# Kernel tuning notes

Measured on AMD Instinct MI355X. Metric: run time of the kernel, lower is better.

The kernel has to match this reference:

```python
import jax, jax.numpy as jnp
import numpy as np

N_NODES = 32768
N_EDGES = 262144
B = 64
FT_IN = 256
HID = 256
HEADS = 4
C = HID // HEADS
FT_OUT = 256
NEG_SLOPE = 0.2


def _lin(k, fi, fo):
    return jax.random.normal(k, (fi, fo), dtype=jnp.float32) / np.sqrt(fi)


def setup_inputs() -> dict:
    key = jax.random.key(0)
    ks = jax.random.split(key, 20)
    x = jax.random.normal(ks[0], (N_NODES, FT_IN), dtype=jnp.float32)
    edge_index = jax.random.randint(ks[1], (2, N_EDGES), 0, N_NODES, dtype=jnp.int64)
    batch = jnp.repeat(jnp.arange(B, dtype=jnp.int64), N_NODES // B)  # sorted segment ids
    return {
        "x": x,
        "edge_index": edge_index,
        "batch": batch,
        "batch_size": B,
        "W1l": _lin(ks[2], FT_IN, HID),
        "W1r": _lin(ks[3], FT_IN, HID),
        "a1": jax.random.normal(ks[4], (HEADS, C), dtype=jnp.float32) / np.sqrt(C),
        "b1": jnp.zeros((HID,), dtype=jnp.float32),
        "W2l": _lin(ks[5], HID, HID),
        "W2r": _lin(ks[6], HID, HID),
        "a2": jax.random.normal(ks[7], (HEADS, C), dtype=jnp.float32) / np.sqrt(C),
        "b2": jnp.zeros((HID,), dtype=jnp.float32),
        "Wm1": _lin(ks[8], HID, 4 * HID),
        "bm1": jnp.zeros((4 * HID,), dtype=jnp.float32),
        "Wm2": _lin(ks[9], 4 * HID, HID),
        "bm2": jnp.zeros((HID,), dtype=jnp.float32),
        "Wf": _lin(ks[10], HID, FT_OUT),
        "bf": jnp.zeros((FT_OUT,), dtype=jnp.float32),
    }


def gatv2_layer(x, src, dst, Wl, Wr, att, bias):
    """PyG GATv2Conv (concat=True, add_self_loops=True, eval-mode dropout)."""
    n = x.shape[0]
    h, c = att.shape
    xl = (x @ Wl).reshape(n, h, c)  # source-side transform (x_j)
    xr = (x @ Wr).reshape(n, h, c)  # target-side transform (x_i)
    loop = jnp.arange(n, dtype=src.dtype)
    s = jnp.concatenate([src, loop])
    d = jnp.concatenate([dst, loop])
    # e_ij = a^T LeakyReLU(Wl x_j + Wr x_i), per head
    e = jax.nn.leaky_relu(xl[s] + xr[d], NEG_SLOPE)  # [E+N, H, C]
    score = jnp.einsum('ehc,hc->eh', e, att)  # [E+N, H]
    # segment softmax over incoming edges of each dst node
    m = jax.ops.segment_max(score, d, num_segments=n)
    ex = jnp.exp(score - m[d])
    denom = jax.ops.segment_sum(ex, d, num_segments=n)
    alpha = ex / denom[d]  # self-loops guarantee denom > 0
    out = jax.ops.segment_sum(alpha[..., None] * xl[s], d, num_segments=n)
    return out.reshape(n, h * c) + bias


def _gelu(x):
    return jax.nn.gelu(x, approximate=False)


def reference(x, edge_index, batch, batch_size,
              W1l, W1r, a1, b1, W2l, W2r, a2, b2,
              Wm1, bm1, Wm2, bm2, Wf, bf):
    src, dst = edge_index[0], edge_index[1]
    h = _gelu(gatv2_layer(x, src, dst, W1l, W1r, a1, b1))
    h = _gelu(gatv2_layer(h, src, dst, W2l, W2r, a2, b2))
    # global mean pool over graphs
    cnt = jax.ops.segment_sum(jnp.ones((h.shape[0],), h.dtype), batch, num_segments=batch_size)
    graph_mean = jax.ops.segment_sum(h, batch, num_segments=batch_size) / cnt[:, None]
    # root node of each graph (node 0 of each contiguous block)
    root = h.reshape(batch_size, -1, h.shape[-1])[:, 0, :]
    z = _gelu(root @ Wm1 + bm1)
    z = _gelu(z @ Wm2 + bm2)
    out = z @ Wf + bf
    return (out, graph_mean)
```

## Files before the change

kernel.cpp:

```cpp
#include <hip/hip_runtime.h>
#include <math.h>

#define NNODES 32768
#define BGRAPH 64
#define NPG 512
#define HID 256

typedef __bf16 bf16x8 __attribute__((ext_vector_type(8)));
typedef float f32x16 __attribute__((ext_vector_type(16)));
typedef unsigned short ushort_t;
typedef unsigned short ushort8v __attribute__((ext_vector_type(8)));
typedef unsigned short ushort4v __attribute__((ext_vector_type(4)));
typedef _Float16 half4v __attribute__((ext_vector_type(4)));

__device__ __forceinline__ float gelu_f(float x) {
  return 0.5f * x * (1.0f + erff(x * 0.70710678118654752440f));
}

__device__ __forceinline__ int swz_off(int r, int k) {
  int kblk = k & ~63;
  int ch = (k >> 3) & 7;
  int slot = ch ^ (r & 7);
  return r * 256 + kblk + (slot << 3) + (k & 7);
}

__device__ __forceinline__ size_t frag_off(int r, int k) {
  return ((size_t)((r >> 5) * 16 + (k >> 4)) << 9) +
         (size_t)(((r & 31) | (((k >> 3) & 1) << 5)) << 3) + (k & 7);
}

__device__ __forceinline__ void gll16(const void* g, void* l) {
  __builtin_amdgcn_global_load_lds(
      (const __attribute__((address_space(1))) unsigned int*)g,
      (__attribute__((address_space(3))) unsigned int*)l, 16, 0, 0);
}

__device__ __forceinline__ float dpp_sum16(float x) {
  int t;
  t = __builtin_amdgcn_update_dpp(0, __builtin_bit_cast(int, x), 0xB1, 0xF, 0xF, true);
  x += __builtin_bit_cast(float, t);
  t = __builtin_amdgcn_update_dpp(0, __builtin_bit_cast(int, x), 0x4E, 0xF, 0xF, true);
  x += __builtin_bit_cast(float, t);
  t = __builtin_amdgcn_update_dpp(0, __builtin_bit_cast(int, x), 0x141, 0xF, 0xF, true);
  x += __builtin_bit_cast(float, t);
  t = __builtin_amdgcn_update_dpp(0, __builtin_bit_cast(int, x), 0x140, 0xF, 0xF, true);
  x += __builtin_bit_cast(float, t);
  return x;
}

__global__ __launch_bounds__(256) void prep_kernel(
    const int* __restrict__ src, const int* __restrict__ dst, int E,
    int* __restrict__ cnt, ushort_t* __restrict__ col_pad,
    const float* __restrict__ W1l, const float* __restrict__ W1r,
    const float* __restrict__ W2l, const float* __restrict__ W2r,
    ushort_t* __restrict__ B1h, ushort_t* __restrict__ B1l,
    ushort_t* __restrict__ B2h, ushort_t* __restrict__ B2l,
    const float* __restrict__ x,
    ushort_t* __restrict__ Xh, ushort_t* __restrict__ Xl) {
  int b = blockIdx.x;
  if (b < 1024) {
    int e = b * 256 + threadIdx.x;
    if (e < E) {
      int d = dst[e];
      int slot = atomicAdd(&cnt[d], 1);
      if (slot < 64) col_pad[(d << 6) | slot] = (ushort_t)src[e];
    }
  } else if (b < 1152) {
    int idx = (b - 1024) * 256 + threadIdx.x;
    int layer = idx >> 14;
    int n = (idx >> 5) & 511;
    int c32 = idx & 31;
    const float* W = layer ? (n < 256 ? W2l : W2r) : (n < 256 ? W1l : W1r);
    int wn = n & 255;
    ushort8v hv, lv;
#pragma unroll
    for (int j = 0; j < 8; ++j) {
      float v = W[(size_t)(c32 * 8 + j) * 256 + wn];
      __bf16 h = (__bf16)v;
      float rem = v - (float)h;
      __bf16 l = (__bf16)rem;
      hv[j] = __builtin_bit_cast(ushort_t, h);
      lv[j] = __builtin_bit_cast(ushort_t, l);
    }
    size_t off = frag_off(n, c32 * 8);
    ushort_t* ho = layer ? B2h : B1h;
    ushort_t* lo = layer ? B2l : B1l;
    *(ushort8v*)(ho + off) = hv;
    *(ushort8v*)(lo + off) = lv;
  } else {
    int idx = (b - 1152) * 256 + threadIdx.x;
    int r = idx >> 5;
    int c32 = idx & 31;
    const float* srcp = x + (size_t)r * 256 + c32 * 8;
    float4 v0 = *(const float4*)srcp;
    float4 v1 = *(const float4*)(srcp + 4);
    float vv[8] = {v0.x, v0.y, v0.z, v0.w, v1.x, v1.y, v1.z, v1.w};
    ushort8v hv, lv;
#pragma unroll
    for (int j = 0; j < 8; ++j) {
      __bf16 h = (__bf16)vv[j];
      float rem = vv[j] - (float)h;
      __bf16 l = (__bf16)rem;
      hv[j] = __builtin_bit_cast(ushort_t, h);
      lv[j] = __builtin_bit_cast(ushort_t, l);
    }
    int off = swz_off(r, c32 * 8);
    *(ushort8v*)(Xh + off) = hv;
    *(ushort8v*)(Xl + off) = lv;
  }
}

__global__ __launch_bounds__(256, 3) void gemm_bf16x3(
    const ushort_t* __restrict__ Ahi, const ushort_t* __restrict__ Alo,
    const ushort_t* __restrict__ Bhi, const ushort_t* __restrict__ Blo,
    _Float16* __restrict__ Cl, float* __restrict__ Cr) {
  __shared__ ushort_t lds[2 * 8192];
  int i = blockIdx.x;
  int xcd = i & 7, slot = i >> 3;
  int bm = (xcd * 32 + (slot >> 2)) * 128;
  int bn = (slot & 3) * 128;

  int tid = threadIdx.x;
  int w = tid >> 6, lane = tid & 63;
  int wm0 = (w >> 1) * 64, wn0 = (w & 1) * 64;
  int r = lane & 31, kg = lane >> 5;
  int cb0 = (bn + wn0) >> 5;

  f32x16 acc[2][2];
#pragma unroll
  for (int mf = 0; mf < 2; ++mf)
#pragma unroll
    for (int nf = 0; nf < 2; ++nf)
#pragma unroll
      for (int e = 0; e < 16; ++e) acc[mf][nf][e] = 0.0f;

  for (int kk = 0; kk < 256; kk += 64) {
#pragma unroll
    for (int t = 0; t < 8; ++t) {
      int tile = t >> 2;
      int q = tid + (t & 3) * 256;
      const ushort_t* gsrc = tile ? Alo : Ahi;
      gll16(gsrc + (size_t)(bm + (q >> 3)) * 256 + kk + (q & 7) * 8,
            lds + tile * 8192 + q * 8);
    }
    __syncthreads();

    int kq0 = kk >> 4;
#pragma unroll
    for (int ks = 0; ks < 4; ++ks) {
      int so = (((ks << 1) | kg) ^ (r & 7)) << 3;
      bf16x8 ah[2], al[2], bh[2], bl[2];
#pragma unroll
      for (int mf = 0; mf < 2; ++mf) {
        int rb = (wm0 + mf * 32 + r) * 64 + so;
        ah[mf] = *(const bf16x8*)(lds + rb);
        al[mf] = *(const bf16x8*)(lds + 8192 + rb);
      }
#pragma unroll
      for (int nf = 0; nf < 2; ++nf) {
        size_t o = ((size_t)((cb0 + nf) * 16 + kq0 + ks) << 9) + (lane << 3);
        bh[nf] = *(const bf16x8*)(Bhi + o);
        bl[nf] = *(const bf16x8*)(Blo + o);
      }
#pragma unroll
      for (int mf = 0; mf < 2; ++mf)
#pragma unroll
        for (int nf = 0; nf < 2; ++nf) {
          acc[mf][nf] = __builtin_amdgcn_mfma_f32_32x32x16_bf16(ah[mf], bh[nf], acc[mf][nf], 0, 0, 0);
          acc[mf][nf] = __builtin_amdgcn_mfma_f32_32x32x16_bf16(ah[mf], bl[nf], acc[mf][nf], 0, 0, 0);
          acc[mf][nf] = __builtin_amdgcn_mfma_f32_32x32x16_bf16(al[mf], bh[nf], acc[mf][nf], 0, 0, 0);
        }
    }
    __syncthreads();
  }

#pragma unroll
  for (int mf = 0; mf < 2; ++mf)
#pragma unroll
    for (int nf = 0; nf < 2; ++nf) {
      int colbase = bn + wn0 + nf * 32;
      int cn = (colbase + r) & 255;
#pragma unroll
      for (int g = 0; g < 16; ++g) {
        int row = bm + wm0 + mf * 32 + (g & 3) + ((g >> 2) << 3) + (kg << 2);
        if (colbase < 256)
          Cl[(size_t)row * 256 + cn] = (_Float16)acc[mf][nf][g];
        else
          Cr[(size_t)row * 256 + cn] = acc[mf][nf][g];
      }
    }
}

__global__ __launch_bounds__(256) void gat_agg(const _Float16* __restrict__ xl,
                                               const float* __restrict__ xr,
                                               const float* __restrict__ att,
                                               const float* __restrict__ bias,
                                               const int* __restrict__ cnt,
                                               const ushort_t* __restrict__ col_pad,
                                               ushort_t* __restrict__ hi_out,
                                               ushort_t* __restrict__ lo_out,
                                               _Float16* __restrict__ h2f16,
                                               float* __restrict__ rootbuf) {
  int wave = (int)((blockIdx.x * (size_t)blockDim.x + threadIdx.x) >> 6);
  int lane = threadIdx.x & 63;
  int d = wave;
  int c0 = lane * 4;
  float4 xr4 = *(const float4*)(xr + (size_t)d * HID + c0);
  float4 a4 = *(const float4*)(att + c0);
  int deg = cnt[d];
  deg = deg < 64 ? deg : 64;
  int mycol = (int)col_pad[(d << 6) + lane];

  auto loadrow = [&](int j) -> float4 {
    int s = (j < deg) ? __builtin_amdgcn_readlane(mycol, j) : d;
    half4v hv = *(const half4v*)(xl + (size_t)s * HID + c0);
    return make_float4((float)hv[0], (float)hv[1], (float)hv[2], (float)hv[3]);
  };

  float l = 0.f, A0 = 0.f, A1 = 0.f, A2 = 0.f, A3 = 0.f;
  float4 v = loadrow(0);
  for (int j = 0; j <= deg; ++j) {
    float4 vc = v;
    if (j < deg) v = loadrow(j + 1);
    float t0 = vc.x + xr4.x, t1 = vc.y + xr4.y, t2 = vc.z + xr4.z, t3 = vc.w + xr4.w;
    t0 = fmaf(0.4f, fabsf(t0), 0.6f * t0);
    t1 = fmaf(0.4f, fabsf(t1), 0.6f * t1);
    t2 = fmaf(0.4f, fabsf(t2), 0.6f * t2);
    t3 = fmaf(0.4f, fabsf(t3), 0.6f * t3);
    float sc = a4.x * t0;
    sc = fmaf(a4.y, t1, sc);
    sc = fmaf(a4.z, t2, sc);
    sc = fmaf(a4.w, t3, sc);
    sc = dpp_sum16(sc);
    float p = __expf(sc);
    l += p;
    A0 = fmaf(p, vc.x, A0);
    A1 = fmaf(p, vc.y, A1);
    A2 = fmaf(p, vc.z, A2);
    A3 = fmaf(p, vc.w, A3);
  }

  float inv = 1.0f / l;
  float v0 = gelu_f(fmaf(A0, inv, bias[c0 + 0]));
  float v1 = gelu_f(fmaf(A1, inv, bias[c0 + 1]));
  float v2 = gelu_f(fmaf(A2, inv, bias[c0 + 2]));
  float v3 = gelu_f(fmaf(A3, inv, bias[c0 + 3]));

  if (hi_out) {
    float vv[4] = {v0, v1, v2, v3};
    ushort4v hv, lv;
#pragma unroll
    for (int j = 0; j < 4; ++j) {
      __bf16 h = (__bf16)vv[j];
      float rem = vv[j] - (float)h;
      __bf16 lb = (__bf16)rem;
      hv[j] = __builtin_bit_cast(ushort_t, h);
      lv[j] = __builtin_bit_cast(ushort_t, lb);
    }
    int off = swz_off(d, c0);
    *(ushort4v*)(hi_out + off) = hv;
    *(ushort4v*)(lo_out + off) = lv;
  }
  if (h2f16) {
    half4v o;
    o[0] = (_Float16)v0; o[1] = (_Float16)v1; o[2] = (_Float16)v2; o[3] = (_Float16)v3;
    *(half4v*)(h2f16 + (size_t)d * HID + c0) = o;
    if ((d & (NPG - 1)) == 0)
      *(float4*)(rootbuf + (size_t)(d >> 9) * HID + c0) = make_float4(v0, v1, v2, v3);
  }
}

__global__ __launch_bounds__(1024) void pool_kernel(const _Float16* __restrict__ h2,
                                                    float* __restrict__ gmean) {
  __shared__ float buf[1024];
  int g = blockIdx.x;
  int q = threadIdx.x >> 8;
  int c = threadIdx.x & 255;
  const _Float16* p = h2 + ((size_t)g * NPG + q * 128) * HID + c;
  float s = 0.f;
#pragma unroll 4
  for (int i = 0; i < 128; ++i) s += (float)p[(size_t)i * HID];
  buf[threadIdx.x] = s;
  __syncthreads();
  if (threadIdx.x < 256) {
    float tot = buf[c] + buf[256 + c] + buf[512 + c] + buf[768 + c];
    gmean[(size_t)g * HID + c] = tot * (1.0f / (float)NPG);
  }
}

__global__ __launch_bounds__(256) void mlp1_kernel(const float* __restrict__ in,
                                                   const float* __restrict__ W,
                                                   const float* __restrict__ b,
                                                   float* __restrict__ outp) {
  __shared__ float s_in[256];
  int g = blockIdx.x >> 2;
  int n0 = (blockIdx.x & 3) * 256;
  const float* row = in + (size_t)g * 256;
  s_in[threadIdx.x] = row[threadIdx.x];
  __syncthreads();
  float acc = 0.f;
  for (int k = 0; k < 256; ++k)
    acc = fmaf(s_in[k], W[(size_t)k * 1024 + n0 + threadIdx.x], acc);
  outp[(size_t)g * 1024 + n0 + threadIdx.x] = gelu_f(acc + b[n0 + threadIdx.x]);
}

__global__ __launch_bounds__(256) void mlp23_kernel(const float* __restrict__ z1,
                                                    const float* __restrict__ Wm2,
                                                    const float* __restrict__ bm2,
                                                    const float* __restrict__ Wf,
                                                    const float* __restrict__ bf,
                                                    float* __restrict__ outp) {
  __shared__ float s1[1024];
  __shared__ float s2[256];
  int g = blockIdx.x;
  int c = threadIdx.x;
  const float* row = z1 + (size_t)g * 1024;
#pragma unroll
  for (int i = 0; i < 4; ++i) s1[c + i * 256] = row[c + i * 256];
  __syncthreads();
  float acc = 0.f;
  for (int k = 0; k < 1024; ++k) acc = fmaf(s1[k], Wm2[(size_t)k * 256 + c], acc);
  s2[c] = gelu_f(acc + bm2[c]);
  __syncthreads();
  float acc2 = 0.f;
  for (int k = 0; k < 256; ++k) acc2 = fmaf(s2[k], Wf[(size_t)k * 256 + c], acc2);
  outp[(size_t)g * 256 + c] = acc2 + bf[c];
}

extern "C" void kernel_launch(void* const* d_in, const int* in_sizes, int n_in,
                              void* d_out, int out_size, void* d_ws, size_t ws_size,
                              hipStream_t stream) {
  const float* x   = (const float*)d_in[0];
  const int* edge  = (const int*)d_in[1];
  const float* W1l = (const float*)d_in[4];
  const float* W1r = (const float*)d_in[5];
  const float* a1  = (const float*)d_in[6];
  const float* b1  = (const float*)d_in[7];
  const float* W2l = (const float*)d_in[8];
  const float* W2r = (const float*)d_in[9];
  const float* a2  = (const float*)d_in[10];
  const float* b2  = (const float*)d_in[11];
  const float* Wm1 = (const float*)d_in[12];
  const float* bm1 = (const float*)d_in[13];
  const float* Wm2 = (const float*)d_in[14];
  const float* bm2 = (const float*)d_in[15];
  const float* Wf  = (const float*)d_in[16];
  const float* bf  = (const float*)d_in[17];
  float* out = (float*)d_out;
  float* gmean = out + BGRAPH * HID;

  const int n = NNODES;
  const int E = in_sizes[1] / 2;
  const int* src = edge;
  const int* dst = edge + E;

  ushort_t* R1h = (ushort_t*)d_ws;
  ushort_t* R1l = R1h + (size_t)n * 256;
  _Float16* h2f16 = (_Float16*)R1h;
  _Float16* xlh = (_Float16*)(R1l + (size_t)n * 256);
  float* xrbuf = (float*)(xlh + (size_t)n * 256);
  float* rootbuf = xrbuf + (size_t)n * 256;
  float* z1 = rootbuf + 64 * 256;
  ushort_t* B1h = (ushort_t*)(z1 + 64 * 1024);
  ushort_t* B1l = B1h + 512 * 256;
  ushort_t* B2h = B1l + 512 * 256;
  ushort_t* B2l = B2h + 512 * 256;
  int* cnt = (int*)(B2l + 512 * 256);
  ushort_t* col_pad = (ushort_t*)(cnt + n);

  hipMemsetAsync(cnt, 0, (size_t)n * sizeof(int), stream);

  prep_kernel<<<1024 + 128 + 4096, 256, 0, stream>>>(
      src, dst, E, cnt, col_pad, W1l, W1r, W2l, W2r,
      B1h, B1l, B2h, B2l, x, R1h, R1l);

  gemm_bf16x3<<<1024, 256, 0, stream>>>(R1h, R1l, B1h, B1l, xlh, xrbuf);
  gat_agg<<<n / 4, 256, 0, stream>>>(xlh, xrbuf, a1, b1, cnt, col_pad,
                                     R1h, R1l, nullptr, nullptr);
  gemm_bf16x3<<<1024, 256, 0, stream>>>(R1h, R1l, B2h, B2l, xlh, xrbuf);
  gat_agg<<<n / 4, 256, 0, stream>>>(xlh, xrbuf, a2, b2, cnt, col_pad,
                                     nullptr, nullptr, h2f16, rootbuf);

  pool_kernel<<<BGRAPH, 1024, 0, stream>>>(h2f16, gmean);
  mlp1_kernel<<<BGRAPH * 4, 256, 0, stream>>>(rootbuf, Wm1, bm1, z1);
  mlp23_kernel<<<BGRAPH, 256, 0, stream>>>(z1, Wm2, bm2, Wf, bf, out);
}
```

Before: 336.6 us.

## Rewrite MLP head as wave-per-output dot products over transposed weights

Transposes the MLP weight matrices in the prep kernel so each output column is a contiguous row. The MLP head is then computed as three kernels with one wavefront per output, each doing a vectorized float4 dot product and a DPP/shuffle reduction. Previously a single thread looped serially over K, and mlp23 ran only 64 blocks, which left most of the GPU idle. The change costs an extra transpose pass over about 2 MB of weights inside prep and one more kernel launch.

```diff
diff --git a/kernel.cpp b/kernel.cpp
--- a/kernel.cpp
+++ b/kernel.cpp
@@ -48,6 +48,13 @@
   return x;
 }
 
+__device__ __forceinline__ float wave_sum64(float x) {
+  x = dpp_sum16(x);
+  x += __shfl_xor(x, 16);
+  x += __shfl_xor(x, 32);
+  return x;
+}
+
 __global__ __launch_bounds__(256) void prep_kernel(
     const int* __restrict__ src, const int* __restrict__ dst, int E,
     int* __restrict__ cnt, ushort_t* __restrict__ col_pad,
@@ -56,7 +63,10 @@
     ushort_t* __restrict__ B1h, ushort_t* __restrict__ B1l,
     ushort_t* __restrict__ B2h, ushort_t* __restrict__ B2l,
     const float* __restrict__ x,
-    ushort_t* __restrict__ Xh, ushort_t* __restrict__ Xl) {
+    ushort_t* __restrict__ Xh, ushort_t* __restrict__ Xl,
+    const float* __restrict__ Wm1, const float* __restrict__ Wm2,
+    const float* __restrict__ Wf,
+    float* __restrict__ W1T, float* __restrict__ W2T, float* __restrict__ WfT) {
   int b = blockIdx.x;
   if (b < 1024) {
     int e = b * 256 + threadIdx.x;
@@ -87,7 +97,7 @@
     ushort_t* lo = layer ? B2l : B1l;
     *(ushort8v*)(ho + off) = hv;
     *(ushort8v*)(lo + off) = lv;
-  } else {
+  } else if (b < 5248) {
     int idx = (b - 1152) * 256 + threadIdx.x;
     int r = idx >> 5;
     int c32 = idx & 31;
@@ -107,6 +117,18 @@
     int off = swz_off(r, c32 * 8);
     *(ushort8v*)(Xh + off) = hv;
     *(ushort8v*)(Xl + off) = lv;
+  } else if (b < 6272) {
+    int idx = (b - 5248) * 256 + threadIdx.x;
+    int k = idx & 255, n = idx >> 8;
+    W1T[(size_t)n * 256 + k] = Wm1[(size_t)k * 1024 + n];
+  } else if (b < 7296) {
+    int idx = (b - 6272) * 256 + threadIdx.x;
+    int k = idx & 1023, c = idx >> 10;
+    W2T[(size_t)c * 1024 + k] = Wm2[(size_t)k * 256 + c];
+  } else {
+    int idx = (b - 7296) * 256 + threadIdx.x;
+    int k = idx & 255, n = idx >> 8;
+    WfT[(size_t)n * 256 + k] = Wf[(size_t)k * 256 + n];
   }
 }
 
@@ -288,43 +310,61 @@
   }
 }
 
-__global__ __launch_bounds__(256) void mlp1_kernel(const float* __restrict__ in,
-                                                   const float* __restrict__ W,
-                                                   const float* __restrict__ b,
-                                                   float* __restrict__ outp) {
-  __shared__ float s_in[256];
-  int g = blockIdx.x >> 2;
-  int n0 = (blockIdx.x & 3) * 256;
-  const float* row = in + (size_t)g * 256;
-  s_in[threadIdx.x] = row[threadIdx.x];
-  __syncthreads();
-  float acc = 0.f;
-  for (int k = 0; k < 256; ++k)
-    acc = fmaf(s_in[k], W[(size_t)k * 1024 + n0 + threadIdx.x], acc);
-  outp[(size_t)g * 1024 + n0 + threadIdx.x] = gelu_f(acc + b[n0 + threadIdx.x]);
-}
-
-__global__ __launch_bounds__(256) void mlp23_kernel(const float* __restrict__ z1,
-                                                    const float* __restrict__ Wm2,
-                                                    const float* __restrict__ bm2,
-                                                    const float* __restrict__ Wf,
-                                                    const float* __restrict__ bf,
-                                                    float* __restrict__ outp) {
-  __shared__ float s1[1024];
-  __shared__ float s2[256];
-  int g = blockIdx.x;
-  int c = threadIdx.x;
-  const float* row = z1 + (size_t)g * 1024;
-#pragma unroll
-  for (int i = 0; i < 4; ++i) s1[c + i * 256] = row[c + i * 256];
-  __syncthreads();
-  float acc = 0.f;
-  for (int k = 0; k < 1024; ++k) acc = fmaf(s1[k], Wm2[(size_t)k * 256 + c], acc);
-  s2[c] = gelu_f(acc + bm2[c]);
-  __syncthreads();
-  float acc2 = 0.f;
-  for (int k = 0; k < 256; ++k) acc2 = fmaf(s2[k], Wf[(size_t)k * 256 + c], acc2);
-  outp[(size_t)g * 256 + c] = acc2 + bf[c];
+__global__ __launch_bounds__(256) void head1(const float* __restrict__ root,
+                                             const float* __restrict__ W1T,
+                                             const float* __restrict__ b1m,
+                                             float* __restrict__ z1) {
+  int wv = (int)((blockIdx.x * 256 + threadIdx.x) >> 6);
+  int lane = threadIdx.x & 63;
+  int g = wv >> 10, nx = wv & 1023;
+  float4 r = *(const float4*)(root + (size_t)g * 256 + lane * 4);
+  float4 w = *(const float4*)(W1T + (size_t)nx * 256 + lane * 4);
+  float p = r.x * w.x;
+  p = fmaf(r.y, w.y, p);
+  p = fmaf(r.z, w.z, p);
+  p = fmaf(r.w, w.w, p);
+  p = wave_sum64(p);
+  if (lane == 0) z1[(size_t)g * 1024 + nx] = gelu_f(p + b1m[nx]);
+}
+
+__global__ __launch_bounds__(256) void head2(const float* __restrict__ z1,
+                                             const float* __restrict__ W2T,
+                                             const float* __restrict__ b2m,
+                                             float* __restrict__ z2) {
+  int wv = (int)((blockIdx.x * 256 + threadIdx.x) >> 6);
+  int lane = threadIdx.x & 63;
+  int g = wv >> 8, c = wv & 255;
+  const float* zr = z1 + (size_t)g * 1024;
+  const float* wr = W2T + (size_t)c * 1024;
+  float p = 0.f;
+#pragma unroll
+  for (int i = 0; i < 4; ++i) {
+    float4 a = *(const float4*)(zr + i * 256 + lane * 4);
+    float4 w = *(const float4*)(wr + i * 256 + lane * 4);
+    p = fmaf(a.x, w.x, p);
+    p = fmaf(a.y, w.y, p);
+    p = fmaf(a.z, w.z, p);
+    p = fmaf(a.w, w.w, p);
+  }
+  p = wave_sum64(p);
+  if (lane == 0) z2[(size_t)g * 256 + c] = gelu_f(p + b2m[c]);
+}
+
+__global__ __launch_bounds__(256) void head3(const float* __restrict__ z2,
+                                             const float* __restrict__ WfT,
+                                             const float* __restrict__ bfm,
+                                             float* __restrict__ outp) {
+  int wv = (int)((blockIdx.x * 256 + threadIdx.x) >> 6);
+  int lane = threadIdx.x & 63;
+  int g = wv >> 8, nx = wv & 255;
+  float4 a = *(const float4*)(z2 + (size_t)g * 256 + lane * 4);
+  float4 w = *(const float4*)(WfT + (size_t)nx * 256 + lane * 4);
+  float p = a.x * w.x;
+  p = fmaf(a.y, w.y, p);
+  p = fmaf(a.z, w.z, p);
+  p = fmaf(a.w, w.w, p);
+  p = wave_sum64(p);
+  if (lane == 0) outp[(size_t)g * 256 + nx] = p + bfm[nx];
 }
 
 extern "C" void kernel_launch(void* const* d_in, const int* in_sizes, int n_in,
@@ -361,18 +401,23 @@
   float* xrbuf = (float*)(xlh + (size_t)n * 256);
   float* rootbuf = xrbuf + (size_t)n * 256;
   float* z1 = rootbuf + 64 * 256;
-  ushort_t* B1h = (ushort_t*)(z1 + 64 * 1024);
+  float* z2 = z1 + 64 * 1024;
+  ushort_t* B1h = (ushort_t*)(z2 + 64 * 256);
   ushort_t* B1l = B1h + 512 * 256;
   ushort_t* B2h = B1l + 512 * 256;
   ushort_t* B2l = B2h + 512 * 256;
   int* cnt = (int*)(B2l + 512 * 256);
   ushort_t* col_pad = (ushort_t*)(cnt + n);
+  float* W1T = (float*)(col_pad + (size_t)n * 64);
+  float* W2T = W1T + 1024 * 256;
+  float* WfT = W2T + 256 * 1024;
 
   hipMemsetAsync(cnt, 0, (size_t)n * sizeof(int), stream);
 
-  prep_kernel<<<1024 + 128 + 4096, 256, 0, stream>>>(
+  prep_kernel<<<7552, 256, 0, stream>>>(
       src, dst, E, cnt, col_pad, W1l, W1r, W2l, W2r,
-      B1h, B1l, B2h, B2l, x, R1h, R1l);
+      B1h, B1l, B2h, B2l, x, R1h, R1l,
+      Wm1, Wm2, Wf, W1T, W2T, WfT);
 
   gemm_bf16x3<<<1024, 256, 0, stream>>>(R1h, R1l, B1h, B1l, xlh, xrbuf);
   gat_agg<<<n / 4, 256, 0, stream>>>(xlh, xrbuf, a1, b1, cnt, col_pad,
@@ -382,6 +427,7 @@
                                      nullptr, nullptr, h2f16, rootbuf);
 
   pool_kernel<<<BGRAPH, 1024, 0, stream>>>(h2f16, gmean);
-  mlp1_kernel<<<BGRAPH * 4, 256, 0, stream>>>(rootbuf, Wm1, bm1, z1);
-  mlp23_kernel<<<BGRAPH, 256, 0, stream>>>(z1, Wm2, bm2, Wf, bf, out);
-}
+  head1<<<BGRAPH * 1024 / 4, 256, 0, stream>>>(rootbuf, W1T, bm1, z1);
+  head2<<<BGRAPH * 256 / 4, 256, 0, stream>>>(z1, W2T, bm2, z2);
+  head3<<<BGRAPH * 256 / 4, 256, 0, stream>>>(z2, WfT, bf, out);
+}
```

Result: faster. 294.6 us (-12.5%).
